# Performance work log

Hardware: AMD Instinct MI355X
Metric: run time of the kernel (lower is better)

Reference implementation:

```python
import jax, jax.numpy as jnp
import numpy as np

DIM = 1024
INTER = 512
E = 32            # n_routed_experts
TOPK = 4          # n_activated_experts
GROUPS = 8        # n_expert_groups
TOPK_GROUPS = 4
SHARED_INTER = 2 * INTER  # n_shared_experts * moe_inter_dim
ROUTE_SCALE = 1.0
B, S = 8, 4096


def setup_inputs() -> dict:
    key = jax.random.key(0)
    ks = jax.random.split(key, 16)
    def xav(k, shape):
        fan_in, fan_out = shape[-2], shape[-1]
        lim = np.sqrt(6.0 / (fan_in + fan_out))
        return jax.random.uniform(k, shape, jnp.float32, -lim, lim)
    return {
        "x": jax.random.normal(ks[0], (B, S, DIM), jnp.float32),
        "gw": xav(ks[1], (DIM, E)),
        "gb": jnp.zeros((E,), jnp.float32),
        "w1": xav(ks[2], (E, DIM, INTER)),
        "b1": jnp.zeros((E, INTER), jnp.float32),
        "w3": xav(ks[3], (E, DIM, INTER)),
        "b3": jnp.zeros((E, INTER), jnp.float32),
        "w2": xav(ks[4], (E, INTER, DIM)),
        "b2": jnp.zeros((E, DIM), jnp.float32),
        "sw1": xav(ks[5], (DIM, SHARED_INTER)),
        "sb1": jnp.zeros((SHARED_INTER,), jnp.float32),
        "sw3": xav(ks[6], (DIM, SHARED_INTER)),
        "sb3": jnp.zeros((SHARED_INTER,), jnp.float32),
        "sw2": xav(ks[7], (SHARED_INTER, DIM)),
        "sb2": jnp.zeros((DIM,), jnp.float32),
    }


def _gate(xf, gw, gb):
    # scores: softmax over routed experts in fp32 (score_func='softmax')
    T = xf.shape[0]
    scores = jax.nn.softmax((xf @ gw + gb).astype(jnp.float32), axis=-1)  # [T, E]
    original_scores = scores
    # group-masked routing (n_expert_groups > 1)
    scores_g = scores.reshape(T, GROUPS, E // GROUPS)                     # [T, G, E/G]
    group_scores = jnp.sum(jax.lax.top_k(scores_g, 2)[0], axis=-1)        # [T, G]
    gidx = jax.lax.top_k(group_scores, TOPK_GROUPS)[1]                    # [T, topk_groups]
    keep = jnp.zeros((T, GROUPS), bool).at[jnp.arange(T)[:, None], gidx].set(True)
    masked = jnp.where(keep[:, :, None], scores_g, -jnp.inf).reshape(T, E)
    indices = jax.lax.top_k(masked, TOPK)[1]                              # [T, topk]
    weights = jnp.take_along_axis(original_scores, indices, axis=1) * ROUTE_SCALE
    return weights.astype(xf.dtype), indices


def reference(x, gw, gb, w1, b1, w3, b3, w2, b2, sw1, sb1, sw3, sb3, sw2, sb2):
    shape = x.shape
    xf = x.reshape(-1, DIM)                                               # [T, dim]
    T = xf.shape[0]
    weights, indices = _gate(xf, gw, gb)
    # dense combine weights [T, E]: w_e(t) = routing weight if expert e chosen for t else 0
    cw = jnp.zeros((T, E), xf.dtype).at[jnp.arange(T)[:, None], indices].add(weights)
    # scan over experts: y += w_e * SwiGLU_e(x). Zero weight -> zero contribution,
    # identical math to the masked dispatch/scatter-add in the torch code.
    def body(y, p):
        w1e, b1e, w3e, b3e, w2e, b2e, we = p
        h = jax.nn.silu(xf @ w1e + b1e) * (xf @ w3e + b3e)                # [T, inter]
        return y + we[:, None] * (h @ w2e + b2e), None
    y0 = jnp.zeros_like(xf)
    y, _ = jax.lax.scan(body, y0, (w1, b1, w3, b3, w2, b2, cw.T))
    # shared experts MLP (SwiGLU)
    z = (jax.nn.silu(xf @ sw1 + sb1) * (xf @ sw3 + sb3)) @ sw2 + sb2
    return (y + z).reshape(shape)
```

## Files before the change

kernel.cpp:

```cpp
#include <hip/hip_runtime.h>
#include <stdint.h>

#define DIM_    1024
#define INTER_  512

typedef short bf16x4 __attribute__((ext_vector_type(4)));
typedef short bf16x8 __attribute__((ext_vector_type(8)));
typedef float f32x4  __attribute__((ext_vector_type(4)));

__device__ __forceinline__ unsigned short f2bf(float f) {
  union { float f; unsigned u; } v; v.f = f;
  return (unsigned short)((v.u + 0x7FFFu + ((v.u >> 16) & 1u)) >> 16);
}
__device__ __forceinline__ unsigned f2bf2(float a, float b) {
  union { float f; unsigned u; } va, vb; va.f = a; vb.f = b;
  unsigned ra = (va.u + 0x7FFFu + ((va.u >> 16) & 1u)) >> 16;
  unsigned rb = (vb.u + 0x7FFFu + ((vb.u >> 16) & 1u)) >> 16;
  return ra | (rb << 16);
}
__device__ __forceinline__ float bfhi(unsigned u) {
  union { unsigned u; float f; } v; v.u = u & 0xffff0000u; return v.f;
}
__device__ __forceinline__ float bflo(unsigned u) {
  union { unsigned u; float f; } v; v.u = u << 16; return v.f;
}

__device__ __forceinline__ void gl16(const void* g, void* l) {
  __builtin_amdgcn_global_load_lds(
      (const __attribute__((address_space(1))) unsigned int*)g,
      (__attribute__((address_space(3))) unsigned int*)l, 16, 0, 0);
}

#define BARX() do { asm volatile("" ::: "memory"); \
                    __builtin_amdgcn_s_barrier();  \
                    asm volatile("" ::: "memory"); } while (0)

__global__ __launch_bounds__(256) void gate_kernel(
    const float* __restrict__ x, const float* __restrict__ gw,
    const float* __restrict__ gb, int* __restrict__ idx, float* __restrict__ wts,
    unsigned short* __restrict__ xb) {
  __shared__ double s_sc[4][32];
  __shared__ double s_gs[4][8];
  const int wid = threadIdx.x >> 6, lane = threadIdx.x & 63;
  const int t = blockIdx.x * 4 + wid;
  {
    const float* xrow = x + (size_t)t * DIM_ + lane * 16;
    unsigned short* xbrow = xb + (size_t)t * DIM_ + lane * 16;
    float4 f0 = *(const float4*)(xrow);
    float4 f1 = *(const float4*)(xrow + 4);
    float4 f2v = *(const float4*)(xrow + 8);
    float4 f3v = *(const float4*)(xrow + 12);
    uint4 o0, o1;
    o0.x = f2bf2(f0.x, f0.y);  o0.y = f2bf2(f0.z, f0.w);
    o0.z = f2bf2(f1.x, f1.y);  o0.w = f2bf2(f1.z, f1.w);
    o1.x = f2bf2(f2v.x, f2v.y); o1.y = f2bf2(f2v.z, f2v.w);
    o1.z = f2bf2(f3v.x, f3v.y); o1.w = f2bf2(f3v.z, f3v.w);
    *(uint4*)(xbrow) = o0;
    *(uint4*)(xbrow + 8) = o1;
  }
  const int e = lane & 31, half = lane >> 5;
  const float* xr  = x  + (size_t)t * DIM_ + half * 512;
  const float* gwp = gw + (size_t)half * 512 * 32 + e;
  double a0 = 0, a1 = 0, a2 = 0, a3 = 0;
  for (int k = 0; k < 512; k += 4) {
    float4 xv = *(const float4*)(xr + k);
    a0 += (double)xv.x * (double)gwp[(k + 0) * 32];
    a1 += (double)xv.y * (double)gwp[(k + 1) * 32];
    a2 += (double)xv.z * (double)gwp[(k + 2) * 32];
    a3 += (double)xv.w * (double)gwp[(k + 3) * 32];
  }
  double lg = (a0 + a1) + (a2 + a3);
  lg += __shfl_xor(lg, 32);
  lg += (double)gb[e];
  double m = lg;
  #pragma unroll
  for (int d = 1; d < 32; d <<= 1) m = fmax(m, __shfl_xor(m, d));
  double ex = exp(lg - m);
  double ssum = ex;
  #pragma unroll
  for (int d = 1; d < 32; d <<= 1) ssum += __shfl_xor(ssum, d);
  double sc = ex / ssum;
  double p  = __shfl_xor(sc, 1);
  double m1 = fmax(sc, p), n1 = fmin(sc, p);
  double m2 = __shfl_xor(m1, 2), n2 = __shfl_xor(n1, 2);
  double gs = (m1 >= m2) ? (m1 + fmax(n1, m2)) : (m2 + fmax(n2, m1));
  if (lane < 32) {
    s_sc[wid][e] = sc;
    if ((e & 3) == 0) s_gs[wid][e >> 2] = gs;
  }
  __syncthreads();
  if (lane == 0) {
    unsigned kmask = 0;
    for (int it = 0; it < 4; ++it) {
      int bg = 0; double bv = -1.0;
      for (int g = 0; g < 8; ++g)
        if (!((kmask >> g) & 1u) && s_gs[wid][g] > bv) { bv = s_gs[wid][g]; bg = g; }
      kmask |= 1u << bg;
    }
    unsigned umask = 0;
    for (int slot = 0; slot < 4; ++slot) {
      int be = 0; double bv = -1.0;
      for (int ee = 0; ee < 32; ++ee)
        if (((kmask >> (ee >> 2)) & 1u) && !((umask >> ee) & 1u) && s_sc[wid][ee] > bv) {
          bv = s_sc[wid][ee]; be = ee;
        }
      umask |= 1u << be;
      idx[t * 4 + slot] = be;
      wts[t * 4 + slot] = (float)bv;
    }
  }
}

__global__ __launch_bounds__(256) void count_kernel(const int* __restrict__ idx,
                                                    int* __restrict__ meta) {
  __shared__ int h[32];
  int tid = threadIdx.x;
  if (tid < 32) h[tid] = 0;
  __syncthreads();
  atomicAdd(&h[idx[blockIdx.x * 256 + tid]], 1);
  __syncthreads();
  if (tid < 32 && h[tid]) atomicAdd(&meta[tid], h[tid]);
}

__global__ void scan_kernel(int* __restrict__ meta) {
  int lane = threadIdx.x & 63;
  if (lane < 32) {
    int c = meta[lane];
    int pre = c;
    #pragma unroll
    for (int d = 1; d < 32; d <<= 1) { int t = __shfl_up(pre, d); if (lane >= d) pre += t; }
    int excl = pre - c;
    meta[64 + lane] = excl;
    meta[32 + lane] = excl;
    int nt = (c + 255) >> 8;
    int ntp = nt;
    #pragma unroll
    for (int d = 1; d < 32; d <<= 1) { int t = __shfl_up(ntp, d); if (lane >= d) ntp += t; }
    int ntExcl = ntp - nt;
    for (int k = 0; k < nt; ++k) { meta[128 + ntExcl + k] = lane; meta[1184 + ntExcl + k] = k << 8; }
    if (lane == 31) { meta[96] = excl + c; meta[97] = ntExcl + nt; }
  }
}

__global__ __launch_bounds__(256) void scatter_kernel(
    const int* __restrict__ idx, int* __restrict__ meta,
    int* __restrict__ tok, int* __restrict__ inv) {
  int i = blockIdx.x * 256 + threadIdx.x;
  int lane = threadIdx.x & 63;
  int e = idx[i];
  unsigned long long m = ~0ull;
  #pragma unroll
  for (int b = 0; b < 5; ++b) {
    unsigned long long vote = __ballot((e >> b) & 1);
    m &= ((e >> b) & 1) ? vote : ~vote;
  }
  int leader = __ffsll((long long)m) - 1;
  int rank = __popcll(m & ((1ull << lane) - 1));
  int base = 0;
  if (lane == leader) base = atomicAdd(&meta[32 + e], (int)__popcll(m));
  base = __shfl(base, leader);
  int p = base + rank;
  tok[p] = i >> 2;
  inv[i] = p;
}

__global__ __launch_bounds__(256) void repack_kernel(
    const float* __restrict__ src, unsigned short* __restrict__ dst,
    int K, int N, int tilesPerMat) {
  const int w = blockIdx.x * 4 + (threadIdx.x >> 6);
  const int j = threadIdx.x & 63;
  const int e = w / tilesPerMat, rem = w % tilesPerMat;
  const int kSteps = K >> 5;
  const int nt = rem / kSteps, kq = rem % kSteps;
  const float* s = src + (size_t)e * K * N + (size_t)(kq * 32) * N + nt * 64 + j;
  float v[32];
  #pragma unroll
  for (int kk = 0; kk < 32; ++kk) v[kk] = s[(size_t)kk * N];
  char* d = (char*)dst + (size_t)w * 4096 + j * 16;
  #pragma unroll
  for (int q = 0; q < 4; ++q) {
    int o = q * 8;
    uint4 tv;
    tv.x = f2bf2(v[o + 0], v[o + 1]);
    tv.y = f2bf2(v[o + 2], v[o + 3]);
    tv.z = f2bf2(v[o + 4], v[o + 5]);
    tv.w = f2bf2(v[o + 6], v[o + 7]);
    *(uint4*)(d + q * 1024) = tv;
  }
}

__global__ __launch_bounds__(256) void repack13_kernel(
    const float* __restrict__ src1, const float* __restrict__ src3,
    unsigned short* __restrict__ dst, int K, int N, int jtTiles) {
  const int w = blockIdx.x * 4 + (threadIdx.x >> 6);
  const int j = threadIdx.x & 63;
  const int kSteps = K >> 5;
  const int tpm = jtTiles * kSteps;
  const int e = w / tpm, rem = w % tpm;
  const int jt = rem / kSteps, kq = rem % kSteps;
  const int jg = jt * 64 + j;
  const int c = ((jg >> 5) << 4) + (jg & 15);
  const float* s = (((jg >> 4) & 1) ? src3 : src1)
                 + (size_t)e * K * N + (size_t)(kq * 32) * N + c;
  float v[32];
  #pragma unroll
  for (int kk = 0; kk < 32; ++kk) v[kk] = s[(size_t)kk * N];
  char* d = (char*)dst + (size_t)w * 4096 + j * 16;
  #pragma unroll
  for (int q = 0; q < 4; ++q) {
    int o = q * 8;
    uint4 tv;
    tv.x = f2bf2(v[o + 0], v[o + 1]);
    tv.y = f2bf2(v[o + 2], v[o + 3]);
    tv.z = f2bf2(v[o + 4], v[o + 5]);
    tv.w = f2bf2(v[o + 6], v[o + 7]);
    *(uint4*)(d + q * 1024) = tv;
  }
}


#define G8_PRE()                                                              \
  const int tid = threadIdx.x, lane = tid & 63, wave = tid >> 6;              \
  const int wm = wave >> 2, wn = wave & 3;                                    \
  const int f = lane & 15, g = lane >> 4;                                     \
  const int wud = wave >> 2, wlo = wave & 3;                                  \
  const int row_in = wlo * 16 + (lane >> 2);                                  \
  const int szr = (row_in & 3) ^ ((row_in >> 2) & 3);                         \
  const int qs = (((lane & 3) ^ szr) << 4);                                   \
  const int btile_off = wlo * 1024 + lane * 16;                               \
  const int wv1k = wave * 1024;                                               \
  const int awb = wm * 8192;                                                  \
  int aoff[4], boff[4];                                                       \
  _Pragma("unroll")                                                           \
  for (int ii = 0; ii < 4; ++ii) {                                            \
    int u16 = ii * 16 + f;                                                    \
    aoff[ii] = u16 * 64 + ((g ^ ((u16 & 3) ^ ((u16 >> 2) & 3))) << 4);        \
    boff[ii] = 16384 + wn * 4096 + g * 1024 + u16 * 16;                       \
  }                                                                           \
  f32x4 acc[8][4];                                                            \
  const f32x4 zz = {0.f, 0.f, 0.f, 0.f};                                      \
  _Pragma("unroll")                                                           \
  for (int mi = 0; mi < 8; ++mi)                                              \
    _Pragma("unroll")                                                         \
    for (int ni = 0; ni < 4; ++ni) acc[mi][ni] = zz;

#define G8_EVEN(s, AFC, AFN, BVC, UMAXv)                                      \
  {                                                                           \
    BARX();                                                                   \
    int u_ = I4 + 3 + (s); if (u_ >= (UMAXv)) u_ = (UMAXv) - 1;               \
    char* td_ = lds + ((((s) + 3) & 3) * 32768);                              \
    gl16(pA0 + u_ * 64, td_ + wv1k);                                          \
    gl16(pA1 + u_ * 64, td_ + 8192 + wv1k);                                   \
    const char* cb_ = lds + (((s) & 3) * 32768);                              \
    _Pragma("unroll")                                                         \
    for (int mi = 0; mi < 4; ++mi)                                            \
      AFN[mi] = *(const bf16x8*)(cb_ + awb + 4096 + aoff[mi]);                \
    __builtin_amdgcn_s_setprio(1);                                            \
    _Pragma("unroll")                                                         \
    for (int ni = 0; ni < 4; ++ni)                                            \
      _Pragma("unroll")                                                       \
      for (int mi = 0; mi < 4; ++mi)                                          \
        acc[mi][ni] = __builtin_amdgcn_mfma_f32_16x16x32_bf16(                \
            AFC[mi], BVC[ni], acc[mi][ni], 0, 0, 0);                          \
    __builtin_amdgcn_s_setprio(0);                                            \
    asm volatile("s_waitcnt vmcnt(6)" ::: "memory");                          \
  }

#define G8_ODD(s, AFC, BVC, AFN, BVN, UMAXv)                                  \
  {                                                                           \
    BARX();                                                                   \
    int u_ = I4 + 3 + (s); if (u_ >= (UMAXv)) u_ = (UMAXv) - 1;               \
    char* td_ = lds + ((((s) + 3) & 3) * 32768);                              \
    gl16(pB0 + (size_t)u_ * 4096, td_ + 16384 + wv1k);                        \
    gl16(pB1 + (size_t)u_ * 4096, td_ + 24576 + wv1k);                        \
    const char* nb_ = lds + ((((s) + 1) & 3) * 32768);                        \
    _Pragma("unroll")                                                         \
    for (int mi = 0; mi < 4; ++mi)                                            \
      AFN[mi] = *(const bf16x8*)(nb_ + awb + aoff[mi]);                       \
    _Pragma("unroll")                                                         \
    for (int ni = 0; ni < 4; ++ni)                                            \
      BVN[ni] = *(const bf16x8*)(nb_ + boff[ni]);                             \
    __builtin_amdgcn_s_setprio(1);                                            \
    _Pragma("unroll")                                                         \
    for (int ni = 0; ni < 4; ++ni)                                            \
      _Pragma("unroll")                                                       \
      for (int mi = 0; mi < 4; ++mi)                                          \
        acc[4 + mi][ni] = __builtin_amdgcn_mfma_f32_16x16x32_bf16(            \
            AFC[mi], BVC[ni], acc[4 + mi][ni], 0, 0, 0);                      \
    __builtin_amdgcn_s_setprio(0);                                            \
  }

#define G8_BODY(UMAXv)                                                        \
  _Pragma("unroll")                                                           \
  for (int uu = 0; uu < 3; ++uu) {                                            \
    gl16(pA0 + uu * 64, lds + uu * 32768 + wv1k);                             \
    gl16(pA1 + uu * 64, lds + uu * 32768 + 8192 + wv1k);                      \
    gl16(pB0 + (size_t)uu * 4096, lds + uu * 32768 + 16384 + wv1k);           \
    gl16(pB1 + (size_t)uu * 4096, lds + uu * 32768 + 24576 + wv1k);           \
  }                                                                           \
  asm volatile("s_waitcnt vmcnt(8)" ::: "memory");                            \
  BARX();                                                                     \
  bf16x8 af0[4], af1[4], bv0[4], bv1[4];                                      \
  _Pragma("unroll")                                                           \
  for (int mi = 0; mi < 4; ++mi)                                              \
    af0[mi] = *(const bf16x8*)(lds + awb + aoff[mi]);                         \
  _Pragma("unroll")                                                           \
  for (int ni = 0; ni < 4; ++ni)                                              \
    bv0[ni] = *(const bf16x8*)(lds + boff[ni]);                               \
  for (int I = 0; I < (UMAXv) / 4; ++I) {                                     \
    const int I4 = I * 4;                                                     \
    G8_EVEN(0, af0, af1, bv0, UMAXv); G8_ODD(0, af1, bv0, af0, bv1, UMAXv);   \
    G8_EVEN(1, af0, af1, bv1, UMAXv); G8_ODD(1, af1, bv1, af0, bv0, UMAXv);   \
    G8_EVEN(2, af0, af1, bv0, UMAXv); G8_ODD(2, af1, bv0, af0, bv1, UMAXv);   \
    G8_EVEN(3, af0, af1, bv1, UMAXv); G8_ODD(3, af1, bv1, af0, bv0, UMAXv);   \
  }

#define XCD_SWZ(GXv)                                                          \
  const int nb_ = gridDim.x;                                                  \
  const int b_ = blockIdx.x;                                                  \
  const int w_ = (b_ & 7) * (nb_ >> 3) + (b_ >> 3);                           \
  const int bx = w_ % (GXv);                                                  \
  const int by = w_ / (GXv);

__global__ __launch_bounds__(512, 2) void s1_kernel(
    const unsigned short* __restrict__ xb, const unsigned short* __restrict__ w13,
    const float* __restrict__ sb1, const float* __restrict__ sb3,
    unsigned short* __restrict__ Hs) {
  __shared__ char lds[131072];
  XCD_SWZ(8);
  const int m0 = by * 256;
  G8_PRE();
  const char* pA0 = (const char*)xb + (size_t)(m0 + wud * 64 + row_in) * 2048 + qs;
  const char* pA1 = pA0 + (size_t)128 * 2048;
  const char* pB0 = (const char*)w13 + ((size_t)(bx * 4 + wud) * 32) * 4096 + btile_off;
  const char* pB1 = (const char*)w13 + ((size_t)(bx * 4 + 2 + wud) * 32) * 4096 + btile_off;
  G8_BODY(32);
  const int colb = bx * 128;
  #pragma unroll
  for (int p2 = 0; p2 < 2; ++p2) {
    int c = colb + wn * 32 + p2 * 16 + f;
    float bb1 = sb1[c], bb3 = sb3[c];
    #pragma unroll
    for (int m8 = 0; m8 < 8; ++m8) {
      int row = m0 + wm * 128 + (m8 >> 2) * 64 + (m8 & 3) * 16 + g * 4;
      #pragma unroll
      for (int r = 0; r < 4; ++r) {
        float v1 = acc[m8][2 * p2][r] + bb1;
        float v3 = acc[m8][2 * p2 + 1][r] + bb3;
        float h = (v1 / (1.f + __expf(-v1))) * v3;
        Hs[(size_t)(row + r) * 1024 + c] = f2bf(h);
      }
    }
  }
}

__global__ __launch_bounds__(512, 2) void s2_kernel(
    const unsigned short* __restrict__ Hs, const unsigned short* __restrict__ b2i,
    const float* __restrict__ sb2, float* __restrict__ out) {
  __shared__ char lds[131072];
  XCD_SWZ(4);
  const int m0 = by * 256;
  G8_PRE();
  const char* pA0 = (const char*)Hs + (size_t)(m0 + wud * 64 + row_in) * 2048 + qs;
  const char* pA1 = pA0 + (size_t)128 * 2048;
  const char* pB0 = (const char*)b2i + ((size_t)(bx * 4 + wud) * 32) * 4096 + btile_off;
  const char* pB1 = (const char*)b2i + ((size_t)(bx * 4 + 2 + wud) * 32) * 4096 + btile_off;
  G8_BODY(32);
  #pragma unroll
  for (int ni = 0; ni < 4; ++ni) {
    int c = bx * 256 + wn * 64 + ni * 16 + f;
    float bb = sb2[c];
    #pragma unroll
    for (int m8 = 0; m8 < 8; ++m8) {
      int row = m0 + wm * 128 + (m8 >> 2) * 64 + (m8 & 3) * 16 + g * 4;
      #pragma unroll
      for (int r = 0; r < 4; ++r)
        out[(size_t)(row + r) * 1024 + c] = acc[m8][ni][r] + bb;
    }
  }
}

__global__ __launch_bounds__(512, 2) void g1_kernel(
    const unsigned short* __restrict__ xb, const unsigned short* __restrict__ w13,
    const float* __restrict__ b1, const float* __restrict__ b3,
    const int* __restrict__ tok, const int* __restrict__ meta,
    unsigned short* __restrict__ H) {
  __shared__ char lds[131072];
  XCD_SWZ(4);
  if (by >= meta[97]) return;
  const int e = meta[128 + by], m0 = meta[1184 + by];
  const int off_e = meta[64 + e], nrem = meta[e] - m0;
  G8_PRE();
  const int r0a = wud * 64 + row_in;
  const int ix0 = off_e + m0 + ((r0a < nrem) ? r0a : 0);
  const int ix1 = off_e + m0 + ((r0a + 128 < nrem) ? r0a + 128 : 0);
  const char* pA0 = (const char*)xb + (size_t)tok[ix0] * 2048 + qs;
  const char* pA1 = (const char*)xb + (size_t)tok[ix1] * 2048 + qs;
  const char* pB0 = (const char*)w13 + ((size_t)(e * 16 + bx * 4 + wud) * 32) * 4096 + btile_off;
  const char* pB1 = (const char*)w13 + ((size_t)(e * 16 + bx * 4 + 2 + wud) * 32) * 4096 + btile_off;
  G8_BODY(32);
  const int colb = bx * 128;
  #pragma unroll
  for (int p2 = 0; p2 < 2; ++p2) {
    int c = colb + wn * 32 + p2 * 16 + f;
    float bb1 = b1[e * 512 + c], bb3 = b3[e * 512 + c];
    #pragma unroll
    for (int m8 = 0; m8 < 8; ++m8) {
      int row = wm * 128 + (m8 >> 2) * 64 + (m8 & 3) * 16 + g * 4;
      #pragma unroll
      for (int r = 0; r < 4; ++r) {
        if (row + r < nrem) {
          float v1 = acc[m8][2 * p2][r] + bb1;
          float v3 = acc[m8][2 * p2 + 1][r] + bb3;
          float h = (v1 / (1.f + __expf(-v1))) * v3;
          H[(size_t)(off_e + m0 + row + r) * 512 + c] = f2bf(h);
        }
      }
    }
  }
}

__global__ __launch_bounds__(512, 2) void g2_kernel(
    const unsigned short* __restrict__ H, const unsigned short* __restrict__ w2i,
    const float* __restrict__ b2, const int* __restrict__ meta,
    unsigned short* __restrict__ Y, int cbase) {
  __shared__ char lds[131072];
  XCD_SWZ(2);
  if (by >= meta[97]) return;
  const int e = meta[128 + by], m0 = meta[1184 + by];
  const int off_e = meta[64 + e], nrem = meta[e] - m0;
  G8_PRE();
  const int r0a = wud * 64 + row_in;
  const int ix0 = off_e + m0 + ((r0a < nrem) ? r0a : 0);
  const int ix1 = off_e + m0 + ((r0a + 128 < nrem) ? r0a + 128 : 0);
  const char* pA0 = (const char*)H + (size_t)ix0 * 1024 + qs;
  const char* pA1 = (const char*)H + (size_t)ix1 * 1024 + qs;
  const int nt0 = (cbase >> 6) + bx * 4;
  const char* pB0 = (const char*)w2i + ((size_t)(e * 16 + nt0 + wud) * 16) * 4096 + btile_off;
  const char* pB1 = (const char*)w2i + ((size_t)(e * 16 + nt0 + 2 + wud) * 16) * 4096 + btile_off;
  G8_BODY(16);
  #pragma unroll
  for (int ni = 0; ni < 4; ++ni) {
    int ycol = bx * 256 + wn * 64 + ni * 16 + f;
    float bb = b2[e * 1024 + cbase + ycol];
    #pragma unroll
    for (int m8 = 0; m8 < 8; ++m8) {
      int row = wm * 128 + (m8 >> 2) * 64 + (m8 & 3) * 16 + g * 4;
      #pragma unroll
      for (int r = 0; r < 4; ++r) {
        if (row + r < nrem)
          Y[(size_t)(off_e + m0 + row + r) * 512 + ycol] = f2bf(acc[m8][ni][r] + bb);
      }
    }
  }
}

__global__ __launch_bounds__(256) void combine_kernel(
    const unsigned short* __restrict__ Y, const int* __restrict__ inv,
    const float* __restrict__ wts, float* __restrict__ out, int cbase) {
  int t = blockIdx.x * 2 + (threadIdx.x >> 7);
  int c = (threadIdx.x & 127) * 4;
  int4 iv = *(const int4*)(inv + t * 4);
  float4 wv = *(const float4*)(wts + t * 4);
  float* op = out + (size_t)t * 1024 + cbase + c;
  float4 o = *(float4*)op;
  uint2 u;
  u = *(const uint2*)(Y + (size_t)iv.x * 512 + c);
  o.x += wv.x * bflo(u.x); o.y += wv.x * bfhi(u.x);
  o.z += wv.x * bflo(u.y); o.w += wv.x * bfhi(u.y);
  u = *(const uint2*)(Y + (size_t)iv.y * 512 + c);
  o.x += wv.y * bflo(u.x); o.y += wv.y * bfhi(u.x);
  o.z += wv.y * bflo(u.y); o.w += wv.y * bfhi(u.y);
  u = *(const uint2*)(Y + (size_t)iv.z * 512 + c);
  o.x += wv.z * bflo(u.x); o.y += wv.z * bfhi(u.x);
  o.z += wv.z * bflo(u.y); o.w += wv.z * bfhi(u.y);
  u = *(const uint2*)(Y + (size_t)iv.w * 512 + c);
  o.x += wv.w * bflo(u.x); o.y += wv.w * bfhi(u.x);
  o.z += wv.w * bflo(u.y); o.w += wv.w * bfhi(u.y);
  *(float4*)op = o;
}

extern "C" void kernel_launch(void* const* d_in, const int* in_sizes, int n_in,
                              void* d_out, int out_size, void* d_ws, size_t ws_size,
                              hipStream_t stream) {
  const float* x   = (const float*)d_in[0];
  const float* gw  = (const float*)d_in[1];
  const float* gb  = (const float*)d_in[2];
  const float* w1  = (const float*)d_in[3];
  const float* b1  = (const float*)d_in[4];
  const float* w3  = (const float*)d_in[5];
  const float* b3  = (const float*)d_in[6];
  const float* w2  = (const float*)d_in[7];
  const float* b2  = (const float*)d_in[8];
  const float* sw1 = (const float*)d_in[9];
  const float* sb1 = (const float*)d_in[10];
  const float* sw3 = (const float*)d_in[11];
  const float* sb3 = (const float*)d_in[12];
  const float* sw2 = (const float*)d_in[13];
  const float* sb2 = (const float*)d_in[14];
  float* out = (float*)d_out;
  char* ws = (char*)d_ws;

  const size_t OFF_XB   = 134217728;
  const size_t OFF_W13I = 201326592;
  const size_t OFF_W2I  = 268435456;
  const size_t OFF_S13I = 301989888;
  const size_t OFF_SW2I = 306184192;
  const size_t OFF_IDX  = 308281344;
  const size_t OFF_WTS  = 308805632;
  const size_t OFF_TOK  = 309329920;
  const size_t OFF_INV  = 309854208;
  const size_t OFF_META = 310378496;
  if (ws_size < OFF_META + 8960) return;

  unsigned short* H    = (unsigned short*)ws;
  unsigned short* xb   = (unsigned short*)(ws + OFF_XB);
  unsigned short* Yb   = (unsigned short*)(ws + OFF_XB);
  unsigned short* w13i = (unsigned short*)(ws + OFF_W13I);
  unsigned short* w2i  = (unsigned short*)(ws + OFF_W2I);
  unsigned short* s13i = (unsigned short*)(ws + OFF_S13I);
  unsigned short* sw2i = (unsigned short*)(ws + OFF_SW2I);
  int*   idx  = (int*)(ws + OFF_IDX);
  float* wts  = (float*)(ws + OFF_WTS);
  int*   tokl = (int*)(ws + OFF_TOK);
  int*   inv  = (int*)(ws + OFF_INV);
  int*   meta = (int*)(ws + OFF_META);

  hipMemsetAsync(meta, 0, 128, stream);
  gate_kernel<<<dim3(8192), dim3(256), 0, stream>>>(x, gw, gb, idx, wts, xb);
  count_kernel<<<dim3(512), dim3(256), 0, stream>>>(idx, meta);
  scan_kernel<<<dim3(1), dim3(64), 0, stream>>>(meta);
  scatter_kernel<<<dim3(512), dim3(256), 0, stream>>>(idx, meta, tokl, inv);
  repack13_kernel<<<dim3(4096), dim3(256), 0, stream>>>(w1, w3, w13i, 1024, 512, 16);
  repack_kernel<<<dim3(2048), dim3(256), 0, stream>>>(w2, w2i, 512, 1024, 256);
  repack13_kernel<<<dim3(256), dim3(256), 0, stream>>>(sw1, sw3, s13i, 1024, 1024, 32);
  repack_kernel<<<dim3(128), dim3(256), 0, stream>>>(sw2, sw2i, 1024, 1024, 512);
  s1_kernel<<<dim3(1024), dim3(512), 0, stream>>>(xb, s13i, sb1, sb3, H);
  s2_kernel<<<dim3(512), dim3(512), 0, stream>>>(H, sw2i, sb2, out);
  g1_kernel<<<dim3(2176), dim3(512), 0, stream>>>(xb, w13i, b1, b3, tokl, meta, H);
  g2_kernel<<<dim3(1088), dim3(512), 0, stream>>>(H, w2i, b2, meta, Yb, 0);
  combine_kernel<<<dim3(16384), dim3(256), 0, stream>>>(Yb, inv, wts, out, 0);
  g2_kernel<<<dim3(1088), dim3(512), 0, stream>>>(H, w2i, b2, meta, Yb, 512);
  combine_kernel<<<dim3(16384), dim3(256), 0, stream>>>(Yb, inv, wts, out, 512);
}
```

Measured before the change: 1.493 ms.

## Halve GEMM N-tile to 256x128 with 3-stage LDS pipeline and higher occupancy

Replaces the 256x256 output tile GEMM macro with a 256x128 tile. Each wave now holds a 4x4 accumulator block instead of 8x4. The software pipeline becomes a simpler 3-buffer ring of 24KB stages, so LDS drops from 128KB to 72KB and launch bounds rise to allow 4 blocks per CU, with grids doubled to match. This trades lower per-block arithmetic intensity and more A-tile reloads (A is re-fetched for twice as many N tiles) for better occupancy and latency hiding. It also drops the interleaved even/odd register double-buffering of fragments.

Result: faster. 1.397 ms (-6.5%).

```diff
diff --git a/kernel.cpp b/kernel.cpp
--- a/kernel.cpp
+++ b/kernel.cpp
@@ -219,100 +219,65 @@
 }
 
 
-#define G8_PRE()                                                              \
+#define G4_PRE()                                                              \
   const int tid = threadIdx.x, lane = tid & 63, wave = tid >> 6;              \
-  const int wm = wave >> 2, wn = wave & 3;                                    \
+  const int wm = wave >> 1, wn = wave & 1;                                    \
   const int f = lane & 15, g = lane >> 4;                                     \
-  const int wud = wave >> 2, wlo = wave & 3;                                  \
-  const int row_in = wlo * 16 + (lane >> 2);                                  \
-  const int szr = (row_in & 3) ^ ((row_in >> 2) & 3);                         \
-  const int qs = (((lane & 3) ^ szr) << 4);                                   \
-  const int btile_off = wlo * 1024 + lane * 16;                               \
+  const int rsg = wave * 16 + (lane >> 2);                                    \
+  const int qs = (((lane & 3) ^ ((rsg & 3) ^ ((rsg >> 2) & 3))) << 4);        \
   const int wv1k = wave * 1024;                                               \
-  const int awb = wm * 8192;                                                  \
+  const int bso = (wave & 3) * 1024 + lane * 16;                              \
   int aoff[4], boff[4];                                                       \
   _Pragma("unroll")                                                           \
   for (int ii = 0; ii < 4; ++ii) {                                            \
     int u16 = ii * 16 + f;                                                    \
-    aoff[ii] = u16 * 64 + ((g ^ ((u16 & 3) ^ ((u16 >> 2) & 3))) << 4);        \
+    aoff[ii] = (wm >> 1) * 8192 + (wm & 1) * 4096 + u16 * 64 +                \
+               ((g ^ ((u16 & 3) ^ ((u16 >> 2) & 3))) << 4);                   \
     boff[ii] = 16384 + wn * 4096 + g * 1024 + u16 * 16;                       \
   }                                                                           \
-  f32x4 acc[8][4];                                                            \
+  f32x4 acc[4][4];                                                            \
   const f32x4 zz = {0.f, 0.f, 0.f, 0.f};                                      \
   _Pragma("unroll")                                                           \
-  for (int mi = 0; mi < 8; ++mi)                                              \
+  for (int mi = 0; mi < 4; ++mi)                                              \
     _Pragma("unroll")                                                         \
     for (int ni = 0; ni < 4; ++ni) acc[mi][ni] = zz;
 
-#define G8_EVEN(s, AFC, AFN, BVC, UMAXv)                                      \
+#define G4_STAGE(td, u_)                                                      \
+  gl16(pA0 + (u_) * 64, (td) + wv1k);                                         \
+  gl16(pA1 + (u_) * 64, (td) + 8192 + wv1k);                                  \
+  gl16(pB + (size_t)(u_) * 4096, (td) + 16384 + wv1k);
+
+#define G4_BODY(NU)                                                           \
   {                                                                           \
+    G4_STAGE(lds, 0);                                                         \
+    G4_STAGE(lds + 24576, ((NU) > 1 ? 1 : 0));                                \
+    asm volatile("s_waitcnt vmcnt(3)" ::: "memory");                          \
     BARX();                                                                   \
-    int u_ = I4 + 3 + (s); if (u_ >= (UMAXv)) u_ = (UMAXv) - 1;               \
-    char* td_ = lds + ((((s) + 3) & 3) * 32768);                              \
-    gl16(pA0 + u_ * 64, td_ + wv1k);                                          \
-    gl16(pA1 + u_ * 64, td_ + 8192 + wv1k);                                   \
-    const char* cb_ = lds + (((s) & 3) * 32768);                              \
+  }                                                                           \
+  int bc = 0, bt = 49152;                                                     \
+  for (int u = 0; u < (NU); ++u) {                                            \
+    const char* cb = lds + bc;                                                \
+    bf16x8 af[4], bv[4];                                                      \
     _Pragma("unroll")                                                         \
-    for (int mi = 0; mi < 4; ++mi)                                            \
-      AFN[mi] = *(const bf16x8*)(cb_ + awb + 4096 + aoff[mi]);                \
+    for (int mi = 0; mi < 4; ++mi) af[mi] = *(const bf16x8*)(cb + aoff[mi]);  \
+    _Pragma("unroll")                                                         \
+    for (int ni = 0; ni < 4; ++ni) bv[ni] = *(const bf16x8*)(cb + boff[ni]);  \
+    int u_ = u + 2; if (u_ > (NU) - 1) u_ = (NU) - 1;                         \
+    char* td = lds + bt;                                                      \
+    G4_STAGE(td, u_);                                                         \
+    BARX();                                                                   \
     __builtin_amdgcn_s_setprio(1);                                            \
     _Pragma("unroll")                                                         \
     for (int ni = 0; ni < 4; ++ni)                                            \
       _Pragma("unroll")                                                       \
       for (int mi = 0; mi < 4; ++mi)                                          \
         acc[mi][ni] = __builtin_amdgcn_mfma_f32_16x16x32_bf16(                \
-            AFC[mi], BVC[ni], acc[mi][ni], 0, 0, 0);                          \
+            af[mi], bv[ni], acc[mi][ni], 0, 0, 0);                            \
     __builtin_amdgcn_s_setprio(0);                                            \
-    asm volatile("s_waitcnt vmcnt(6)" ::: "memory");                          \
-  }
-
-#define G8_ODD(s, AFC, BVC, AFN, BVN, UMAXv)                                  \
-  {                                                                           \
+    asm volatile("s_waitcnt vmcnt(3)" ::: "memory");                          \
     BARX();                                                                   \
-    int u_ = I4 + 3 + (s); if (u_ >= (UMAXv)) u_ = (UMAXv) - 1;               \
-    char* td_ = lds + ((((s) + 3) & 3) * 32768);                              \
-    gl16(pB0 + (size_t)u_ * 4096, td_ + 16384 + wv1k);                        \
-    gl16(pB1 + (size_t)u_ * 4096, td_ + 24576 + wv1k);                        \
-    const char* nb_ = lds + ((((s) + 1) & 3) * 32768);                        \
-    _Pragma("unroll")                                                         \
-    for (int mi = 0; mi < 4; ++mi)                                            \
-      AFN[mi] = *(const bf16x8*)(nb_ + awb + aoff[mi]);                       \
-    _Pragma("unroll")                                                         \
-    for (int ni = 0; ni < 4; ++ni)                                            \
-      BVN[ni] = *(const bf16x8*)(nb_ + boff[ni]);                             \
-    __builtin_amdgcn_s_setprio(1);                                            \
-    _Pragma("unroll")                                                         \
-    for (int ni = 0; ni < 4; ++ni)                                            \
-      _Pragma("unroll")                                                       \
-      for (int mi = 0; mi < 4; ++mi)                                          \
-        acc[4 + mi][ni] = __builtin_amdgcn_mfma_f32_16x16x32_bf16(            \
-            AFC[mi], BVC[ni], acc[4 + mi][ni], 0, 0, 0);                      \
-    __builtin_amdgcn_s_setprio(0);                                            \
-  }
-
-#define G8_BODY(UMAXv)                                                        \
-  _Pragma("unroll")                                                           \
-  for (int uu = 0; uu < 3; ++uu) {                                            \
-    gl16(pA0 + uu * 64, lds + uu * 32768 + wv1k);                             \
-    gl16(pA1 + uu * 64, lds + uu * 32768 + 8192 + wv1k);                      \
-    gl16(pB0 + (size_t)uu * 4096, lds + uu * 32768 + 16384 + wv1k);           \
-    gl16(pB1 + (size_t)uu * 4096, lds + uu * 32768 + 24576 + wv1k);           \
-  }                                                                           \
-  asm volatile("s_waitcnt vmcnt(8)" ::: "memory");                            \
-  BARX();                                                                     \
-  bf16x8 af0[4], af1[4], bv0[4], bv1[4];                                      \
-  _Pragma("unroll")                                                           \
-  for (int mi = 0; mi < 4; ++mi)                                              \
-    af0[mi] = *(const bf16x8*)(lds + awb + aoff[mi]);                         \
-  _Pragma("unroll")                                                           \
-  for (int ni = 0; ni < 4; ++ni)                                              \
-    bv0[ni] = *(const bf16x8*)(lds + boff[ni]);                               \
-  for (int I = 0; I < (UMAXv) / 4; ++I) {                                     \
-    const int I4 = I * 4;                                                     \
-    G8_EVEN(0, af0, af1, bv0, UMAXv); G8_ODD(0, af1, bv0, af0, bv1, UMAXv);   \
-    G8_EVEN(1, af0, af1, bv1, UMAXv); G8_ODD(1, af1, bv1, af0, bv0, UMAXv);   \
-    G8_EVEN(2, af0, af1, bv0, UMAXv); G8_ODD(2, af1, bv0, af0, bv1, UMAXv);   \
-    G8_EVEN(3, af0, af1, bv1, UMAXv); G8_ODD(3, af1, bv1, af0, bv0, UMAXv);   \
+    bc = (bc == 49152) ? 0 : bc + 24576;                                      \
+    bt = (bt == 49152) ? 0 : bt + 24576;                                      \
   }
 
 #define XCD_SWZ(GXv)                                                          \
@@ -322,31 +287,30 @@
   const int bx = w_ % (GXv);                                                  \
   const int by = w_ / (GXv);
 
-__global__ __launch_bounds__(512, 2) void s1_kernel(
+__global__ __launch_bounds__(512, 4) void s1_kernel(
     const unsigned short* __restrict__ xb, const unsigned short* __restrict__ w13,
     const float* __restrict__ sb1, const float* __restrict__ sb3,
     unsigned short* __restrict__ Hs) {
-  __shared__ char lds[131072];
-  XCD_SWZ(8);
+  __shared__ char lds[73728];
+  XCD_SWZ(16);
   const int m0 = by * 256;
-  G8_PRE();
-  const char* pA0 = (const char*)xb + (size_t)(m0 + wud * 64 + row_in) * 2048 + qs;
+  G4_PRE();
+  const char* pA0 = (const char*)xb + (size_t)(m0 + rsg) * 2048 + qs;
   const char* pA1 = pA0 + (size_t)128 * 2048;
-  const char* pB0 = (const char*)w13 + ((size_t)(bx * 4 + wud) * 32) * 4096 + btile_off;
-  const char* pB1 = (const char*)w13 + ((size_t)(bx * 4 + 2 + wud) * 32) * 4096 + btile_off;
-  G8_BODY(32);
-  const int colb = bx * 128;
+  const char* pB = (const char*)w13 + ((size_t)(bx * 2 + (wave >> 2)) * 32) * 4096 + bso;
+  G4_BODY(32);
+  const int colb = bx * 64;
   #pragma unroll
   for (int p2 = 0; p2 < 2; ++p2) {
     int c = colb + wn * 32 + p2 * 16 + f;
     float bb1 = sb1[c], bb3 = sb3[c];
     #pragma unroll
-    for (int m8 = 0; m8 < 8; ++m8) {
-      int row = m0 + wm * 128 + (m8 >> 2) * 64 + (m8 & 3) * 16 + g * 4;
+    for (int mi = 0; mi < 4; ++mi) {
+      int row = m0 + wm * 64 + mi * 16 + g * 4;
       #pragma unroll
       for (int r = 0; r < 4; ++r) {
-        float v1 = acc[m8][2 * p2][r] + bb1;
-        float v3 = acc[m8][2 * p2 + 1][r] + bb3;
+        float v1 = acc[mi][2 * p2][r] + bb1;
+        float v3 = acc[mi][2 * p2 + 1][r] + bb3;
         float h = (v1 / (1.f + __expf(-v1))) * v3;
         Hs[(size_t)(row + r) * 1024 + c] = f2bf(h);
       }
@@ -354,64 +318,61 @@
   }
 }
 
-__global__ __launch_bounds__(512, 2) void s2_kernel(
+__global__ __launch_bounds__(512, 4) void s2_kernel(
     const unsigned short* __restrict__ Hs, const unsigned short* __restrict__ b2i,
     const float* __restrict__ sb2, float* __restrict__ out) {
-  __shared__ char lds[131072];
-  XCD_SWZ(4);
+  __shared__ char lds[73728];
+  XCD_SWZ(8);
   const int m0 = by * 256;
-  G8_PRE();
-  const char* pA0 = (const char*)Hs + (size_t)(m0 + wud * 64 + row_in) * 2048 + qs;
+  G4_PRE();
+  const char* pA0 = (const char*)Hs + (size_t)(m0 + rsg) * 2048 + qs;
   const char* pA1 = pA0 + (size_t)128 * 2048;
-  const char* pB0 = (const char*)b2i + ((size_t)(bx * 4 + wud) * 32) * 4096 + btile_off;
-  const char* pB1 = (const char*)b2i + ((size_t)(bx * 4 + 2 + wud) * 32) * 4096 + btile_off;
-  G8_BODY(32);
+  const char* pB = (const char*)b2i + ((size_t)(bx * 2 + (wave >> 2)) * 32) * 4096 + bso;
+  G4_BODY(32);
   #pragma unroll
   for (int ni = 0; ni < 4; ++ni) {
-    int c = bx * 256 + wn * 64 + ni * 16 + f;
+    int c = bx * 128 + wn * 64 + ni * 16 + f;
     float bb = sb2[c];
     #pragma unroll
-    for (int m8 = 0; m8 < 8; ++m8) {
-      int row = m0 + wm * 128 + (m8 >> 2) * 64 + (m8 & 3) * 16 + g * 4;
+    for (int mi = 0; mi < 4; ++mi) {
+      int row = m0 + wm * 64 + mi * 16 + g * 4;
       #pragma unroll
       for (int r = 0; r < 4; ++r)
-        out[(size_t)(row + r) * 1024 + c] = acc[m8][ni][r] + bb;
+        out[(size_t)(row + r) * 1024 + c] = acc[mi][ni][r] + bb;
     }
   }
 }
 
-__global__ __launch_bounds__(512, 2) void g1_kernel(
+__global__ __launch_bounds__(512, 4) void g1_kernel(
     const unsigned short* __restrict__ xb, const unsigned short* __restrict__ w13,
     const float* __restrict__ b1, const float* __restrict__ b3,
     const int* __restrict__ tok, const int* __restrict__ meta,
     unsigned short* __restrict__ H) {
-  __shared__ char lds[131072];
-  XCD_SWZ(4);
+  __shared__ char lds[73728];
+  XCD_SWZ(8);
   if (by >= meta[97]) return;
   const int e = meta[128 + by], m0 = meta[1184 + by];
   const int off_e = meta[64 + e], nrem = meta[e] - m0;
-  G8_PRE();
-  const int r0a = wud * 64 + row_in;
-  const int ix0 = off_e + m0 + ((r0a < nrem) ? r0a : 0);
-  const int ix1 = off_e + m0 + ((r0a + 128 < nrem) ? r0a + 128 : 0);
+  G4_PRE();
+  const int ix0 = off_e + m0 + ((rsg < nrem) ? rsg : 0);
+  const int ix1 = off_e + m0 + ((rsg + 128 < nrem) ? rsg + 128 : 0);
   const char* pA0 = (const char*)xb + (size_t)tok[ix0] * 2048 + qs;
   const char* pA1 = (const char*)xb + (size_t)tok[ix1] * 2048 + qs;
-  const char* pB0 = (const char*)w13 + ((size_t)(e * 16 + bx * 4 + wud) * 32) * 4096 + btile_off;
-  const char* pB1 = (const char*)w13 + ((size_t)(e * 16 + bx * 4 + 2 + wud) * 32) * 4096 + btile_off;
-  G8_BODY(32);
-  const int colb = bx * 128;
+  const char* pB = (const char*)w13 + ((size_t)(e * 16 + bx * 2 + (wave >> 2)) * 32) * 4096 + bso;
+  G4_BODY(32);
+  const int colb = bx * 64;
   #pragma unroll
   for (int p2 = 0; p2 < 2; ++p2) {
     int c = colb + wn * 32 + p2 * 16 + f;
     float bb1 = b1[e * 512 + c], bb3 = b3[e * 512 + c];
     #pragma unroll
-    for (int m8 = 0; m8 < 8; ++m8) {
-      int row = wm * 128 + (m8 >> 2) * 64 + (m8 & 3) * 16 + g * 4;
+    for (int mi = 0; mi < 4; ++mi) {
+      int row = wm * 64 + mi * 16 + g * 4;
       #pragma unroll
       for (int r = 0; r < 4; ++r) {
         if (row + r < nrem) {
-          float v1 = acc[m8][2 * p2][r] + bb1;
-          float v3 = acc[m8][2 * p2 + 1][r] + bb3;
+          float v1 = acc[mi][2 * p2][r] + bb1;
+          float v3 = acc[mi][2 * p2 + 1][r] + bb3;
           float h = (v1 / (1.f + __expf(-v1))) * v3;
           H[(size_t)(off_e + m0 + row + r) * 512 + c] = f2bf(h);
         }
@@ -420,36 +381,34 @@
   }
 }
 
-__global__ __launch_bounds__(512, 2) void g2_kernel(
+__global__ __launch_bounds__(512, 4) void g2_kernel(
     const unsigned short* __restrict__ H, const unsigned short* __restrict__ w2i,
     const float* __restrict__ b2, const int* __restrict__ meta,
     unsigned short* __restrict__ Y, int cbase) {
-  __shared__ char lds[131072];
-  XCD_SWZ(2);
+  __shared__ char lds[73728];
+  XCD_SWZ(4);
   if (by >= meta[97]) return;
   const int e = meta[128 + by], m0 = meta[1184 + by];
   const int off_e = meta[64 + e], nrem = meta[e] - m0;
-  G8_PRE();
-  const int r0a = wud * 64 + row_in;
-  const int ix0 = off_e + m0 + ((r0a < nrem) ? r0a : 0);
-  const int ix1 = off_e + m0 + ((r0a + 128 < nrem) ? r0a + 128 : 0);
+  G4_PRE();
+  const int ix0 = off_e + m0 + ((rsg < nrem) ? rsg : 0);
+  const int ix1 = off_e + m0 + ((rsg + 128 < nrem) ? rsg + 128 : 0);
   const char* pA0 = (const char*)H + (size_t)ix0 * 1024 + qs;
   const char* pA1 = (const char*)H + (size_t)ix1 * 1024 + qs;
-  const int nt0 = (cbase >> 6) + bx * 4;
-  const char* pB0 = (const char*)w2i + ((size_t)(e * 16 + nt0 + wud) * 16) * 4096 + btile_off;
-  const char* pB1 = (const char*)w2i + ((size_t)(e * 16 + nt0 + 2 + wud) * 16) * 4096 + btile_off;
-  G8_BODY(16);
+  const int nt0 = (cbase >> 6) + bx * 2;
+  const char* pB = (const char*)w2i + ((size_t)(e * 16 + nt0 + (wave >> 2)) * 16) * 4096 + bso;
+  G4_BODY(16);
   #pragma unroll
   for (int ni = 0; ni < 4; ++ni) {
-    int ycol = bx * 256 + wn * 64 + ni * 16 + f;
+    int ycol = bx * 128 + wn * 64 + ni * 16 + f;
     float bb = b2[e * 1024 + cbase + ycol];
     #pragma unroll
-    for (int m8 = 0; m8 < 8; ++m8) {
-      int row = wm * 128 + (m8 >> 2) * 64 + (m8 & 3) * 16 + g * 4;
+    for (int mi = 0; mi < 4; ++mi) {
+      int row = wm * 64 + mi * 16 + g * 4;
       #pragma unroll
       for (int r = 0; r < 4; ++r) {
         if (row + r < nrem)
-          Y[(size_t)(off_e + m0 + row + r) * 512 + ycol] = f2bf(acc[m8][ni][r] + bb);
+          Y[(size_t)(off_e + m0 + row + r) * 512 + ycol] = f2bf(acc[mi][ni][r] + bb);
       }
     }
   }
@@ -535,11 +494,11 @@
   repack_kernel<<<dim3(2048), dim3(256), 0, stream>>>(w2, w2i, 512, 1024, 256);
   repack13_kernel<<<dim3(256), dim3(256), 0, stream>>>(sw1, sw3, s13i, 1024, 1024, 32);
   repack_kernel<<<dim3(128), dim3(256), 0, stream>>>(sw2, sw2i, 1024, 1024, 512);
-  s1_kernel<<<dim3(1024), dim3(512), 0, stream>>>(xb, s13i, sb1, sb3, H);
-  s2_kernel<<<dim3(512), dim3(512), 0, stream>>>(H, sw2i, sb2, out);
-  g1_kernel<<<dim3(2176), dim3(512), 0, stream>>>(xb, w13i, b1, b3, tokl, meta, H);
-  g2_kernel<<<dim3(1088), dim3(512), 0, stream>>>(H, w2i, b2, meta, Yb, 0);
+  s1_kernel<<<dim3(2048), dim3(512), 0, stream>>>(xb, s13i, sb1, sb3, H);
+  s2_kernel<<<dim3(1024), dim3(512), 0, stream>>>(H, sw2i, sb2, out);
+  g1_kernel<<<dim3(4352), dim3(512), 0, stream>>>(xb, w13i, b1, b3, tokl, meta, H);
+  g2_kernel<<<dim3(2176), dim3(512), 0, stream>>>(H, w2i, b2, meta, Yb, 0);
   combine_kernel<<<dim3(16384), dim3(256), 0, stream>>>(Yb, inv, wts, out, 0);
-  g2_kernel<<<dim3(1088), dim3(512), 0, stream>>>(H, w2i, b2, meta, Yb, 512);
+  g2_kernel<<<dim3(2176), dim3(512), 0, stream>>>(H, w2i, b2, meta, Yb, 512);
   combine_kernel<<<dim3(16384), dim3(256), 0, stream>>>(Yb, inv, wts, out, 512);
 }
```
